# Performance work log

Hardware: AMD Instinct MI355X
Metric: run time of the kernel (lower is better)

## Reference

```python
import jax, jax.numpy as jnp
import numpy as np

N_NODES = 100000


def leaky(x):
    return jax.nn.leaky_relu(x, negative_slope=0.01)


def gcn_conv(h, W, b, src, dst, n_nodes):
    """PyG GCNConv: add self-loops, symmetric deg^{-1/2} normalization, scatter-add."""
    h = h @ W  # [N, out]
    deg = jax.ops.segment_sum(jnp.ones_like(dst, dtype=h.dtype), dst, num_segments=n_nodes) + 1.0  # +1 self-loop
    dinv = jax.lax.rsqrt(deg)  # deg >= 1 always
    norm = dinv[src] * dinv[dst]  # [E]
    msg = h[src] * norm[:, None]  # gather + scale, [E, out]
    agg = jax.ops.segment_sum(msg, dst, num_segments=n_nodes)
    agg = agg + h * (dinv * dinv)[:, None]  # self-loop message
    return agg + b


def setup_inputs() -> dict:
    key = jax.random.key(0)
    ks = jax.random.split(key, 16)
    num_teams = 100000
    n_edges = 5000000
    n_matches = 1000000
    x = jax.random.randint(ks[0], (N_NODES, 1), 0, num_teams)
    edge_index = jax.random.randint(ks[1], (2, n_edges), 0, N_NODES)
    home = jax.random.randint(ks[2], (n_matches,), 0, N_NODES)
    away = jax.random.randint(ks[3], (n_matches,), 0, N_NODES)
    emb = jax.random.normal(ks[4], (num_teams, 3), dtype=jnp.float32)
    W1 = jax.random.normal(ks[5], (3, 16), dtype=jnp.float32) * (1.0 / np.sqrt(3))
    b1 = jnp.zeros((16,), dtype=jnp.float32)
    W2 = jax.random.normal(ks[6], (16, 3), dtype=jnp.float32) * 0.25
    b2 = jnp.zeros((3,), dtype=jnp.float32)
    lw1 = jax.random.normal(ks[7], (6, 16), dtype=jnp.float32) * (1.0 / np.sqrt(6))
    lb1 = jnp.zeros((16,), dtype=jnp.float32)
    lw2 = jax.random.normal(ks[8], (16, 6), dtype=jnp.float32) * 0.25
    lb2 = jnp.zeros((6,), dtype=jnp.float32)
    lw3 = jax.random.normal(ks[9], (6, 3), dtype=jnp.float32) * (1.0 / np.sqrt(6))
    lb3 = jnp.zeros((3,), dtype=jnp.float32)
    return dict(x=x, edge_index=edge_index, home=home, away=away, emb=emb,
                W1=W1, b1=b1, W2=W2, b2=b2,
                lw1=lw1, lb1=lb1, lw2=lw2, lb2=lb2, lw3=lw3, lb3=lb3)


def reference(x, edge_index, home, away, emb, W1, b1, W2, b2, lw1, lb1, lw2, lb2, lw3, lb3):
    src, dst = edge_index[0], edge_index[1]
    h = emb[x[:, 0]]  # embedding lookup + squeeze(1) -> [N, 3]
    h = leaky(gcn_conv(h, W1, b1, src, dst, N_NODES))  # [N, 16]
    h = leaky(gcn_conv(h, W2, b2, src, dst, N_NODES))  # [N, 3]
    z = jnp.concatenate([h[home], h[away]], axis=-1)  # [M, 6]
    z = leaky(z @ lw1 + lb1)
    z = leaky(z @ lw2 + lb2)
    z = leaky(z @ lw3 + lb3)
    return z.reshape(-1, 3)
```

## Files before the change

kernel.cpp:

```cpp
#include <hip/hip_runtime.h>

typedef unsigned int u32;
typedef unsigned short u16;

static __device__ __forceinline__ float leaky(float v) {
    return v >= 0.0f ? v : 0.01f * v;
}

#define P1_CHUNK 8192
#define P1_T 256
#define NBK 512
#define P2_T 256
#define ASPLIT 4
#define SBLK 1024
#define S1F 8388608.0f
#define S2F 2097152.0f

static __device__ __forceinline__ int ghat(const int* __restrict__ gh,
                                           const int* __restrict__ bsum,
                                           int i, int ghN, int nE) {
    return (i == ghN) ? nE : gh[i] + bsum[i >> 10];
}

__global__ void k_p1hist(const int* __restrict__ dst, int* __restrict__ gh,
                         int nE, int nb) {
    __shared__ int hist[NBK];
    int t = threadIdx.x;
    hist[t] = 0; hist[t + 256] = 0;
    __syncthreads();
    int base = blockIdx.x * P1_CHUNK;
    int lim = min(P1_CHUNK, nE - base);
    if (lim == P1_CHUNK) {
        const int4* p = (const int4*)(dst + base);
        for (int i = t; i < P1_CHUNK / 4; i += P1_T) {
            int4 v = p[i];
            atomicAdd(&hist[v.x >> 8], 1);
            atomicAdd(&hist[v.y >> 8], 1);
            atomicAdd(&hist[v.z >> 8], 1);
            atomicAdd(&hist[v.w >> 8], 1);
        }
    } else {
        for (int i = t; i < lim; i += P1_T)
            atomicAdd(&hist[dst[base + i] >> 8], 1);
    }
    __syncthreads();
    gh[t * nb + blockIdx.x] = hist[t];
    gh[(t + 256) * nb + blockIdx.x] = hist[t + 256];
}

__global__ void g_scanA(const int* __restrict__ in, int* __restrict__ out,
                        int* __restrict__ bsum, int n) {
    __shared__ int s[SBLK];
    int t = threadIdx.x, i = blockIdx.x * SBLK + t;
    int v = (i < n) ? in[i] : 0;
    s[t] = v;
    for (int o = 1; o < SBLK; o <<= 1) {
        __syncthreads();
        int x = (t >= o) ? s[t - o] : 0;
        __syncthreads();
        s[t] += x;
    }
    __syncthreads();
    if (i < n) out[i] = s[t] - v;
    if (t == SBLK - 1) bsum[blockIdx.x] = s[t];
}
__global__ void g_scanB(int* __restrict__ bsum, int nb) {
    __shared__ int s[SBLK];
    int t = threadIdx.x;
    int v = (t < nb) ? bsum[t] : 0;
    s[t] = v;
    for (int o = 1; o < SBLK; o <<= 1) {
        __syncthreads();
        int x = (t >= o) ? s[t - o] : 0;
        __syncthreads();
        s[t] += x;
    }
    __syncthreads();
    if (t < nb) bsum[t] = s[t] - v;
}
__global__ void g_scanC(int* __restrict__ out, const int* __restrict__ bsum,
                        int n, int total) {
    int i = blockIdx.x * blockDim.x + threadIdx.x;
    if (i < n) out[i] += bsum[i / SBLK];
    if (i == 0) out[n] = total;
}

__global__ __launch_bounds__(256) void k_p1scatter(
        const int* __restrict__ src, const int* __restrict__ dst,
        const int* __restrict__ gh, const int* __restrict__ bsum,
        u32* __restrict__ bkt, int nE, int nb, int ghN) {
    __shared__ int cur[NBK];
    __shared__ int loff[NBK];
    __shared__ int gb[NBK];
    __shared__ int sc[NBK];
    __shared__ u32 pay[P1_CHUNK];
    __shared__ u16 bb[P1_CHUNK];
    int t = threadIdx.x;
    int blk = blockIdx.x;
    int idx0 = t * nb + blk;
    int idx1 = (t + 256) * nb + blk;
    int g0 = ghat(gh, bsum, idx0, ghN, nE);
    int c0 = ghat(gh, bsum, idx0 + 1, ghN, nE) - g0;
    int g1 = ghat(gh, bsum, idx1, ghN, nE);
    int c1 = ghat(gh, bsum, idx1 + 1, ghN, nE) - g1;
    gb[t] = g0; gb[t + 256] = g1;
    sc[t] = c0; sc[t + 256] = c1;
    for (int o = 1; o < NBK; o <<= 1) {
        __syncthreads();
        int a0 = (t >= o) ? sc[t - o] : 0;
        int a1 = (t + 256 >= o) ? sc[t + 256 - o] : 0;
        __syncthreads();
        sc[t] += a0; sc[t + 256] += a1;
    }
    __syncthreads();
    loff[t] = sc[t] - c0;           loff[t + 256] = sc[t + 256] - c1;
    cur[t] = loff[t];               cur[t + 256] = loff[t + 256];
    __syncthreads();
    int base = blk * P1_CHUNK;
    int lim = min(P1_CHUNK, nE - base);
    int n4 = lim >> 2;
    const int4* d4p = (const int4*)(dst + base);
    const int4* s4p = (const int4*)(src + base);
    for (int i = t; i < n4; i += P1_T) {
        int4 d4 = d4p[i];
        int4 s4 = s4p[i];
        int b, r;
        b = d4.x >> 8; r = atomicAdd(&cur[b], 1);
        pay[r] = (u32)(((d4.x & 255) << 17) | s4.x); bb[r] = (u16)b;
        b = d4.y >> 8; r = atomicAdd(&cur[b], 1);
        pay[r] = (u32)(((d4.y & 255) << 17) | s4.y); bb[r] = (u16)b;
        b = d4.z >> 8; r = atomicAdd(&cur[b], 1);
        pay[r] = (u32)(((d4.z & 255) << 17) | s4.z); bb[r] = (u16)b;
        b = d4.w >> 8; r = atomicAdd(&cur[b], 1);
        pay[r] = (u32)(((d4.w & 255) << 17) | s4.w); bb[r] = (u16)b;
    }
    for (int i = (n4 << 2) + t; i < lim; i += P1_T) {
        int d = dst[base + i], s = src[base + i];
        int b = d >> 8;
        int r = atomicAdd(&cur[b], 1);
        pay[r] = (u32)(((d & 255) << 17) | s);
        bb[r] = (u16)b;
    }
    __syncthreads();
    for (int i = t; i < lim; i += P1_T) {
        int b = bb[i];
        bkt[gb[b] + (i - loff[b])] = pay[i];
    }
}

__global__ void k_cnt1(const u32* __restrict__ bkt, const int* __restrict__ gh,
                       const int* __restrict__ bsum,
                       const int* __restrict__ x, const float* __restrict__ emb,
                       float* __restrict__ dinv, float4* __restrict__ hd0,
                       int nE, int nb, int ghN, int nN) {
    __shared__ int h[256];
    int t = threadIdx.x, b = blockIdx.x;
    int base = ghat(gh, bsum, b * nb, ghN, nE);
    int end  = (b + 1 < NBK) ? ghat(gh, bsum, (b + 1) * nb, ghN, nE) : nE;
    h[t] = 0;
    __syncthreads();
    int a0 = min((base + 3) & ~3, end);
    if (base + t < a0) atomicAdd(&h[bkt[base + t] >> 17], 1);
    int vend = a0 + ((end - a0) & ~3);
    for (int i = a0 + t * 4; i < vend; i += P2_T * 4) {
        uint4 v = *(const uint4*)&bkt[i];
        atomicAdd(&h[v.x >> 17], 1);
        atomicAdd(&h[v.y >> 17], 1);
        atomicAdd(&h[v.z >> 17], 1);
        atomicAdd(&h[v.w >> 17], 1);
    }
    if (vend + t < end) atomicAdd(&h[bkt[vend + t] >> 17], 1);
    __syncthreads();
    int d = b * 256 + t;
    if (d < nN) {
        float di = rsqrtf((float)h[t] + 1.0f);
        dinv[d] = di;
        int xi = x[d] * 3;
        hd0[d] = make_float4(emb[xi] * di, emb[xi + 1] * di, emb[xi + 2] * di, 0.f);
    }
}

__global__ __launch_bounds__(256) void k_aggI(
        const u32* __restrict__ bkt, const int* __restrict__ gh,
        const int* __restrict__ bsum,
        const float4* __restrict__ tab, float* __restrict__ pacc,
        int nE, int nb, int ghN, float scale, float inv_scale) {
    __shared__ int acc[768];
    int t = threadIdx.x;
    int blk = blockIdx.x, b = blk >> 2, s = blk & 3;
    int base = ghat(gh, bsum, b * nb, ghN, nE);
    int end  = (b + 1 < NBK) ? ghat(gh, bsum, (b + 1) * nb, ghN, nE) : nE;
    int sz = end - base;
    int chunk = (sz + ASPLIT - 1) / ASPLIT;
    int st = min(base + s * chunk, end);
    int en = min(st + chunk, end);
    acc[t] = 0; acc[t + 256] = 0; acc[t + 512] = 0;
    __syncthreads();
    int a0 = min((st + 3) & ~3, en);
    if (st + t < a0) {
        u32 v = bkt[st + t];
        float4 h = tab[v & 0x1FFFFu];
        int bin = (int)(v >> 17) * 3;
        atomicAdd(&acc[bin + 0], __float2int_rn(h.x * scale));
        atomicAdd(&acc[bin + 1], __float2int_rn(h.y * scale));
        atomicAdd(&acc[bin + 2], __float2int_rn(h.z * scale));
    }
    int vend = a0 + ((en - a0) & ~3);
    for (int i = a0 + t * 4; i < vend; i += P2_T * 4) {
        uint4 v = *(const uint4*)&bkt[i];
        float4 h0 = tab[v.x & 0x1FFFFu];
        float4 h1 = tab[v.y & 0x1FFFFu];
        float4 h2 = tab[v.z & 0x1FFFFu];
        float4 h3 = tab[v.w & 0x1FFFFu];
        int b0 = (int)(v.x >> 17) * 3, b1 = (int)(v.y >> 17) * 3;
        int b2 = (int)(v.z >> 17) * 3, b3 = (int)(v.w >> 17) * 3;
        atomicAdd(&acc[b0 + 0], __float2int_rn(h0.x * scale));
        atomicAdd(&acc[b0 + 1], __float2int_rn(h0.y * scale));
        atomicAdd(&acc[b0 + 2], __float2int_rn(h0.z * scale));
        atomicAdd(&acc[b1 + 0], __float2int_rn(h1.x * scale));
        atomicAdd(&acc[b1 + 1], __float2int_rn(h1.y * scale));
        atomicAdd(&acc[b1 + 2], __float2int_rn(h1.z * scale));
        atomicAdd(&acc[b2 + 0], __float2int_rn(h2.x * scale));
        atomicAdd(&acc[b2 + 1], __float2int_rn(h2.y * scale));
        atomicAdd(&acc[b2 + 2], __float2int_rn(h2.z * scale));
        atomicAdd(&acc[b3 + 0], __float2int_rn(h3.x * scale));
        atomicAdd(&acc[b3 + 1], __float2int_rn(h3.y * scale));
        atomicAdd(&acc[b3 + 2], __float2int_rn(h3.z * scale));
    }
    if (vend + t < en) {
        u32 v = bkt[vend + t];
        float4 h = tab[v & 0x1FFFFu];
        int bin = (int)(v >> 17) * 3;
        atomicAdd(&acc[bin + 0], __float2int_rn(h.x * scale));
        atomicAdd(&acc[bin + 1], __float2int_rn(h.y * scale));
        atomicAdd(&acc[bin + 2], __float2int_rn(h.z * scale));
    }
    __syncthreads();
    float* p = pacc + (size_t)blk * 768;
    p[t]       = (float)acc[t * 3 + 0] * inv_scale;
    p[t + 256] = (float)acc[t * 3 + 1] * inv_scale;
    p[t + 512] = (float)acc[t * 3 + 2] * inv_scale;
}

__global__ void k_fin1(const float* __restrict__ pacc, const float* __restrict__ dinv,
                       const float4* __restrict__ hd0,
                       const float* __restrict__ W1, const float* __restrict__ b1,
                       const float* __restrict__ W2,
                       float4* __restrict__ hd2, int nN) {
    int d = blockIdx.x * blockDim.x + threadIdx.x;
    if (d >= nN) return;
    int b = d >> 8, q = d & 255;
    float s0 = 0.f, s1 = 0.f, s2 = 0.f;
#pragma unroll
    for (int s = 0; s < ASPLIT; ++s) {
        const float* p = pacc + (size_t)(b * ASPLIT + s) * 768;
        s0 += p[q]; s1 += p[q + 256]; s2 += p[q + 512];
    }
    float di = dinv[d];
    float4 self = hd0[d];
    float a0 = di * (s0 + self.x);
    float a1 = di * (s1 + self.y);
    float a2 = di * (s2 + self.z);
    float o0 = 0.f, o1 = 0.f, o2 = 0.f;
#pragma unroll
    for (int k = 0; k < 16; ++k) {
        float p = leaky(a0 * W1[k] + a1 * W1[16 + k] + a2 * W1[32 + k] + b1[k]);
        o0 += p * W2[k * 3 + 0];
        o1 += p * W2[k * 3 + 1];
        o2 += p * W2[k * 3 + 2];
    }
    hd2[d] = make_float4(o0 * di, o1 * di, o2 * di, 0.f);
}

__global__ void k_fin2(const float* __restrict__ pacc, const float* __restrict__ dinv,
                       const float4* __restrict__ hd2, const float* __restrict__ b2,
                       float4* __restrict__ h2, int nN) {
    int d = blockIdx.x * blockDim.x + threadIdx.x;
    if (d >= nN) return;
    int b = d >> 8, q = d & 255;
    float s0 = 0.f, s1 = 0.f, s2 = 0.f;
#pragma unroll
    for (int s = 0; s < ASPLIT; ++s) {
        const float* p = pacc + (size_t)(b * ASPLIT + s) * 768;
        s0 += p[q]; s1 += p[q + 256]; s2 += p[q + 512];
    }
    float di = dinv[d];
    float4 self = hd2[d];
    h2[d] = make_float4(leaky(di * (s0 + self.x) + b2[0]),
                        leaky(di * (s1 + self.y) + b2[1]),
                        leaky(di * (s2 + self.z) + b2[2]), 0.f);
}

__global__ __launch_bounds__(256) void k_mlp4v(
        const int* __restrict__ home, const int* __restrict__ away,
        const float4* __restrict__ h2,
        const float* __restrict__ lw1, const float* __restrict__ lb1,
        const float* __restrict__ lw2, const float* __restrict__ lb2,
        const float* __restrict__ lw3, const float* __restrict__ lb3,
        float* __restrict__ out, int nM) {
    __shared__ float s[235];
    int t = threadIdx.x;
    if (t < 96)       s[t] = lw1[t];
    else if (t < 112) s[t] = lb1[t - 96];
    else if (t < 208) s[t] = lw2[t - 112];
    else if (t < 214) s[t] = lb2[t - 208];
    else if (t < 232) s[t] = lw3[t - 214];
    else if (t < 235) s[t] = lb3[t - 232];
    __syncthreads();
    const float* sw1 = s;        const float* sb1 = s + 96;
    const float* sw2 = s + 112;  const float* sb2 = s + 208;
    const float* sw3 = s + 214;  const float* sb3 = s + 232;

    int i = blockIdx.x * blockDim.x + threadIdx.x;
    int m0 = i * 4;
    if (m0 >= nM) return;
    float res[12];
    int nq = min(4, nM - m0);
    int hidx[4], aidx[4];
    if (nq == 4) {
        int4 hv = *(const int4*)&home[m0];
        int4 av = *(const int4*)&away[m0];
        hidx[0] = hv.x; hidx[1] = hv.y; hidx[2] = hv.z; hidx[3] = hv.w;
        aidx[0] = av.x; aidx[1] = av.y; aidx[2] = av.z; aidx[3] = av.w;
    } else {
        for (int j = 0; j < nq; ++j) { hidx[j] = home[m0 + j]; aidx[j] = away[m0 + j]; }
    }
    for (int j = 0; j < nq; ++j) {
        float4 zh = h2[hidx[j]];
        float4 za = h2[aidx[j]];
        float z[6] = {zh.x, zh.y, zh.z, za.x, za.y, za.z};
        float t1[16];
#pragma unroll
        for (int k = 0; k < 16; ++k) {
            float p = sb1[k];
#pragma unroll
            for (int q = 0; q < 6; ++q) p += z[q] * sw1[q * 16 + k];
            t1[k] = leaky(p);
        }
        float t2[6];
#pragma unroll
        for (int k = 0; k < 6; ++k) {
            float p = sb2[k];
#pragma unroll
            for (int q = 0; q < 16; ++q) p += t1[q] * sw2[q * 6 + k];
            t2[k] = leaky(p);
        }
#pragma unroll
        for (int k = 0; k < 3; ++k) {
            float p = sb3[k];
#pragma unroll
            for (int q = 0; q < 6; ++q) p += t2[q] * sw3[q * 3 + k];
            res[j * 3 + k] = leaky(p);
        }
    }
    if (nq == 4) {
        float4* o4 = (float4*)&out[m0 * 3];
        o4[0] = make_float4(res[0], res[1], res[2], res[3]);
        o4[1] = make_float4(res[4], res[5], res[6], res[7]);
        o4[2] = make_float4(res[8], res[9], res[10], res[11]);
    } else {
        for (int j = 0; j < nq * 3; ++j) out[m0 * 3 + j] = res[j];
    }
}

__global__ void k_hist(const int* __restrict__ dst, int* __restrict__ cnt, int nE) {
    int e = blockIdx.x * blockDim.x + threadIdx.x;
    if (e < nE) atomicAdd(&cnt[dst[e]], 1);
}
__global__ void k_prep(const int* __restrict__ off, const int* __restrict__ cnt,
                       float* __restrict__ dinv, int* __restrict__ cur, int nN) {
    int i = blockIdx.x * blockDim.x + threadIdx.x;
    if (i >= nN) return;
    dinv[i] = rsqrtf((float)cnt[i] + 1.0f);
    cur[i] = off[i];
}
__global__ void k_hd0(const int* __restrict__ x, const float* __restrict__ emb,
                      const float* __restrict__ dinv, float4* __restrict__ hd0, int nN) {
    int i = blockIdx.x * blockDim.x + threadIdx.x;
    if (i >= nN) return;
    float di = dinv[i];
    int xi = x[i] * 3;
    hd0[i] = make_float4(emb[xi] * di, emb[xi + 1] * di, emb[xi + 2] * di, 0.0f);
}
__global__ void k_place(const int* __restrict__ src, const int* __restrict__ dst,
                        int* __restrict__ cur, int* __restrict__ csr, int nE) {
    int e = blockIdx.x * blockDim.x + threadIdx.x;
    if (e >= nE) return;
    int p = atomicAdd(&cur[dst[e]], 1);
    csr[p] = src[e];
}
__global__ void k_gather1w(const int* __restrict__ off, const int* __restrict__ csr,
                           const float4* __restrict__ hd0, const float* __restrict__ dinv,
                           const float* __restrict__ W1, const float* __restrict__ b1,
                           const float* __restrict__ W2,
                           float4* __restrict__ hd2, int nN) {
    int g = blockIdx.x * blockDim.x + threadIdx.x;
    int d = g >> 6, lane = threadIdx.x & 63;
    if (d >= nN) return;
    int e0 = off[d], e1 = off[d + 1];
    float sx = 0.f, sy = 0.f, sz = 0.f;
    for (int e = e0 + lane; e < e1; e += 64) {
        float4 v = hd0[csr[e]];
        sx += v.x; sy += v.y; sz += v.z;
    }
    for (int o = 32; o; o >>= 1) {
        sx += __shfl_down(sx, o);
        sy += __shfl_down(sy, o);
        sz += __shfl_down(sz, o);
    }
    if (lane == 0) {
        float di = dinv[d];
        float4 self = hd0[d];
        float a0 = di * (sx + self.x);
        float a1 = di * (sy + self.y);
        float a2 = di * (sz + self.z);
        float o0 = 0.f, o1 = 0.f, o2 = 0.f;
#pragma unroll
        for (int k = 0; k < 16; ++k) {
            float p = leaky(a0 * W1[k] + a1 * W1[16 + k] + a2 * W1[32 + k] + b1[k]);
            o0 += p * W2[k * 3 + 0];
            o1 += p * W2[k * 3 + 1];
            o2 += p * W2[k * 3 + 2];
        }
        hd2[d] = make_float4(o0 * di, o1 * di, o2 * di, 0.0f);
    }
}
__global__ void k_gather2(const int* __restrict__ off, const int* __restrict__ csr,
                          const float4* __restrict__ hd2, const float* __restrict__ dinv,
                          const float* __restrict__ b2,
                          float4* __restrict__ h2, int nN) {
    int g = blockIdx.x * blockDim.x + threadIdx.x;
    int d = g >> 4, lane = threadIdx.x & 15;
    if (d >= nN) return;
    int e0 = off[d], e1 = off[d + 1];
    float s0 = 0.f, s1 = 0.f, s2 = 0.f;
    for (int e = e0 + lane; e < e1; e += 16) {
        float4 v = hd2[csr[e]];
        s0 += v.x; s1 += v.y; s2 += v.z;
    }
    for (int o = 8; o; o >>= 1) {
        s0 += __shfl_down(s0, o, 16);
        s1 += __shfl_down(s1, o, 16);
        s2 += __shfl_down(s2, o, 16);
    }
    if (lane == 0) {
        float di = dinv[d];
        float4 self = hd2[d];
        h2[d] = make_float4(leaky(di * (s0 + self.x) + b2[0]),
                            leaky(di * (s1 + self.y) + b2[1]),
                            leaky(di * (s2 + self.z) + b2[2]), 0.f);
    }
}

extern "C" void kernel_launch(void* const* d_in, const int* in_sizes, int n_in,
                              void* d_out, int out_size, void* d_ws, size_t ws_size,
                              hipStream_t stream) {
    const int*   x    = (const int*)d_in[0];
    const int*   ei   = (const int*)d_in[1];
    const int*   home = (const int*)d_in[2];
    const int*   away = (const int*)d_in[3];
    const float* emb  = (const float*)d_in[4];
    const float* W1   = (const float*)d_in[5];
    const float* b1   = (const float*)d_in[6];
    const float* W2   = (const float*)d_in[7];
    const float* b2   = (const float*)d_in[8];
    const float* lw1  = (const float*)d_in[9];
    const float* lb1  = (const float*)d_in[10];
    const float* lw2  = (const float*)d_in[11];
    const float* lb2  = (const float*)d_in[12];
    const float* lw3  = (const float*)d_in[13];
    const float* lb3  = (const float*)d_in[14];
    float* out = (float*)d_out;

    const int nN = in_sizes[0];
    const int nE = in_sizes[1] / 2;
    const int nM = in_sizes[2];
    const int* src = ei;
    const int* dst = ei + nE;
    const int B = 256;

    const int nb1 = (nE + P1_CHUNK - 1) / P1_CHUNK;
    const int ghN = NBK * nb1;
    const int nbs = (ghN + SBLK - 1) / SBLK;
    const size_t paccN = (size_t)NBK * ASPLIT * 768;

    size_t need = (size_t)3 * nN * 16 + (size_t)nE * 4 + (size_t)(ghN + 1) * 4 +
                  paccN * 4 + (size_t)nN * 4 + (size_t)(nbs + 8) * 4;

    if (nN <= NBK * 256 && ws_size >= need && nbs <= SBLK) {
        char* w = (char*)d_ws;
        float4* hd0 = (float4*)w;                 w += (size_t)nN * 16;
        float4* hd2 = (float4*)w;                 w += (size_t)nN * 16;
        float4* h2  = (float4*)w;                 w += (size_t)nN * 16;
        u32* bkt  = (u32*)w;                      w += (size_t)nE * 4;
        float* pacc = (float*)w;                  w += paccN * 4;
        int* gh   = (int*)w;                      w += (size_t)(ghN + 1) * 4;
        float* dinv = (float*)w;                  w += (size_t)nN * 4;
        int* bsum = (int*)w;

        k_p1hist<<<nb1, P1_T, 0, stream>>>(dst, gh, nE, nb1);
        g_scanA<<<nbs, SBLK, 0, stream>>>(gh, gh, bsum, ghN);
        g_scanB<<<1, SBLK, 0, stream>>>(bsum, nbs);
        k_p1scatter<<<nb1, P1_T, 0, stream>>>(src, dst, gh, bsum, bkt, nE, nb1, ghN);
        k_cnt1<<<NBK, P2_T, 0, stream>>>(bkt, gh, bsum, x, emb, dinv, hd0,
                                         nE, nb1, ghN, nN);
        k_aggI<<<NBK * ASPLIT, P2_T, 0, stream>>>(bkt, gh, bsum, hd0, pacc,
                                                  nE, nb1, ghN, S1F, 1.0f / S1F);
        k_fin1<<<(nN + B - 1) / B, B, 0, stream>>>(pacc, dinv, hd0, W1, b1, W2,
                                                   hd2, nN);
        k_aggI<<<NBK * ASPLIT, P2_T, 0, stream>>>(bkt, gh, bsum, hd2, pacc,
                                                  nE, nb1, ghN, S2F, 1.0f / S2F);
        k_fin2<<<(nN + B - 1) / B, B, 0, stream>>>(pacc, dinv, hd2, b2, h2, nN);
        int nQuads = (nM + 3) / 4;
        k_mlp4v<<<(nQuads + B - 1) / B, B, 0, stream>>>(home, away, h2,
                                                        lw1, lb1, lw2, lb2, lw3, lb3,
                                                        out, nM);
    } else {
        char* w = (char*)d_ws;
        float4* hd0 = (float4*)w;                 w += (size_t)nN * 16;
        float4* hd2 = (float4*)w;                 w += (size_t)nN * 16;
        float4* h2  = (float4*)w;                 w += (size_t)nN * 16;
        int* csr  = (int*)w;                      w += (size_t)nE * 4;
        int* cnt  = (int*)w;                      w += (size_t)(nN + 1) * 4;
        int* off  = (int*)w;                      w += (size_t)(nN + 1) * 4;
        int* cur  = (int*)w;                      w += (size_t)nN * 4;
        float* dinv = (float*)w;                  w += (size_t)nN * 4;
        int* bsum = (int*)w;

        const int nTot = nN + 1;
        const int nbScan = (nTot + SBLK - 1) / SBLK;

        hipMemsetAsync(cnt, 0, (size_t)nTot * sizeof(int), stream);
        k_hist<<<(nE + B - 1) / B, B, 0, stream>>>(dst, cnt, nE);
        g_scanA<<<nbScan, SBLK, 0, stream>>>(cnt, off, bsum, nTot);
        g_scanB<<<1, SBLK, 0, stream>>>(bsum, nbScan);
        g_scanC<<<(nTot + B - 1) / B, B, 0, stream>>>(off, bsum, nTot - 1, nE);
        k_prep<<<(nN + B - 1) / B, B, 0, stream>>>(off, cnt, dinv, cur, nN);
        k_hd0<<<(nN + B - 1) / B, B, 0, stream>>>(x, emb, dinv, hd0, nN);
        k_place<<<(nE + B - 1) / B, B, 0, stream>>>(src, dst, cur, csr, nE);
        k_gather1w<<<((size_t)nN * 64 + B - 1) / B, B, 0, stream>>>(off, csr, hd0, dinv,
                                                                    W1, b1, W2, hd2, nN);
        k_gather2<<<((size_t)nN * 16 + B - 1) / B, B, 0, stream>>>(off, csr, hd2,
                                                                   dinv, b2, h2, nN);
        int nQuads = (nM + 3) / 4;
        k_mlp4v<<<(nQuads + B - 1) / B, B, 0, stream>>>(home, away, h2,
                                                        lw1, lb1, lw2, lb2, lw3, lb3,
                                                        out, nM);
    }
}
```

Measured before the change: 136.9 us.

## Fuse degree, both GCN aggregations and MLP into one cooperative persistent kernel

Replaces the chain of degree-count, two aggregation, two finalize and MLP kernels with a single cooperative kernel of 512 blocks, separated by grid syncs. Each block stages its bucket's edges in LDS once and reuses them across the degree pass and both aggregation passes. Partial-accumulator round trips through global memory and the extra launches go away. In exchange each bucket runs on one block instead of four splits, so parallelism drops and LDS use rises, and grid-wide barriers are added. The fallback path also loses its uint4 vectorized loads, and the CSR fallback branch is removed.

```diff
diff --git a/kernel.cpp b/kernel.cpp
--- a/kernel.cpp
+++ b/kernel.cpp
@@ -1,4 +1,7 @@
 #include <hip/hip_runtime.h>
+#include <hip/hip_cooperative_groups.h>
+
+namespace cg = cooperative_groups;
 
 typedef unsigned int u32;
 typedef unsigned short u16;
@@ -13,6 +16,7 @@
 #define P2_T 256
 #define ASPLIT 4
 #define SBLK 1024
+#define STG_CAP 14336
 #define S1F 8388608.0f
 #define S2F 2097152.0f
 
@@ -77,12 +81,6 @@
     }
     __syncthreads();
     if (t < nb) bsum[t] = s[t] - v;
-}
-__global__ void g_scanC(int* __restrict__ out, const int* __restrict__ bsum,
-                        int n, int total) {
-    int i = blockIdx.x * blockDim.x + threadIdx.x;
-    if (i < n) out[i] += bsum[i / SBLK];
-    if (i == 0) out[n] = total;
 }
 
 __global__ __launch_bounds__(256) void k_p1scatter(
@@ -148,6 +146,183 @@
     }
 }
 
+__global__ __launch_bounds__(256, 2) void k_mega(
+        const u32* __restrict__ bkt, const int* __restrict__ gh,
+        const int* __restrict__ bsum,
+        const int* __restrict__ x, const float* __restrict__ emb,
+        const float* __restrict__ W1, const float* __restrict__ b1,
+        const float* __restrict__ W2, const float* __restrict__ b2,
+        const int* __restrict__ home, const int* __restrict__ away,
+        const float* __restrict__ lw1, const float* __restrict__ lb1,
+        const float* __restrict__ lw2, const float* __restrict__ lb2,
+        const float* __restrict__ lw3, const float* __restrict__ lb3,
+        float4* hd0, float4* hd2, float4* h2, float* __restrict__ out,
+        int nE, int nb, int ghN, int nN, int nM) {
+    cg::grid_group grid = cg::this_grid();
+    __shared__ u32 stg[STG_CAP];
+    __shared__ int acc[768];
+    __shared__ float mw[235];
+    int t = threadIdx.x, b = blockIdx.x;
+    int base = ghat(gh, bsum, b * nb, ghN, nE);
+    int end  = (b + 1 < NBK) ? ghat(gh, bsum, (b + 1) * nb, ghN, nE) : nE;
+    int sz = end - base;
+    bool fits = (sz <= STG_CAP);
+
+    if (fits) for (int i = t; i < sz; i += 256) stg[i] = bkt[base + i];
+
+    acc[t] = 0;
+    __syncthreads();
+    if (fits) { for (int i = t; i < sz; i += 256) atomicAdd(&acc[stg[i] >> 17], 1); }
+    else      { for (int i = t; i < sz; i += 256) atomicAdd(&acc[bkt[base + i] >> 17], 1); }
+    __syncthreads();
+    int deg = acc[t];
+    float di = rsqrtf((float)deg + 1.0f);
+    int d = b * 256 + t;
+    float4 self = make_float4(0.f, 0.f, 0.f, 0.f);
+    if (d < nN) {
+        int xi = x[d] * 3;
+        self = make_float4(emb[xi] * di, emb[xi + 1] * di, emb[xi + 2] * di, 0.f);
+        hd0[d] = self;
+    }
+    grid.sync();
+
+    acc[t] = 0; acc[t + 256] = 0; acc[t + 512] = 0;
+    __syncthreads();
+    if (fits) {
+        for (int i = t; i < sz; i += 256) {
+            u32 v = stg[i];
+            float4 h = hd0[v & 0x1FFFFu];
+            int bin = (int)(v >> 17) * 3;
+            atomicAdd(&acc[bin + 0], __float2int_rn(h.x * S1F));
+            atomicAdd(&acc[bin + 1], __float2int_rn(h.y * S1F));
+            atomicAdd(&acc[bin + 2], __float2int_rn(h.z * S1F));
+        }
+    } else {
+        for (int i = t; i < sz; i += 256) {
+            u32 v = bkt[base + i];
+            float4 h = hd0[v & 0x1FFFFu];
+            int bin = (int)(v >> 17) * 3;
+            atomicAdd(&acc[bin + 0], __float2int_rn(h.x * S1F));
+            atomicAdd(&acc[bin + 1], __float2int_rn(h.y * S1F));
+            atomicAdd(&acc[bin + 2], __float2int_rn(h.z * S1F));
+        }
+    }
+    __syncthreads();
+    float4 self2 = make_float4(0.f, 0.f, 0.f, 0.f);
+    if (d < nN) {
+        float s0 = (float)acc[t * 3 + 0] * (1.0f / S1F);
+        float s1 = (float)acc[t * 3 + 1] * (1.0f / S1F);
+        float s2 = (float)acc[t * 3 + 2] * (1.0f / S1F);
+        float a0 = di * (s0 + self.x);
+        float a1 = di * (s1 + self.y);
+        float a2 = di * (s2 + self.z);
+        float o0 = 0.f, o1 = 0.f, o2 = 0.f;
+#pragma unroll
+        for (int k = 0; k < 16; ++k) {
+            float p = leaky(a0 * W1[k] + a1 * W1[16 + k] + a2 * W1[32 + k] + b1[k]);
+            o0 += p * W2[k * 3 + 0];
+            o1 += p * W2[k * 3 + 1];
+            o2 += p * W2[k * 3 + 2];
+        }
+        self2 = make_float4(o0 * di, o1 * di, o2 * di, 0.f);
+        hd2[d] = self2;
+    }
+    grid.sync();
+
+    acc[t] = 0; acc[t + 256] = 0; acc[t + 512] = 0;
+    __syncthreads();
+    if (fits) {
+        for (int i = t; i < sz; i += 256) {
+            u32 v = stg[i];
+            float4 h = hd2[v & 0x1FFFFu];
+            int bin = (int)(v >> 17) * 3;
+            atomicAdd(&acc[bin + 0], __float2int_rn(h.x * S2F));
+            atomicAdd(&acc[bin + 1], __float2int_rn(h.y * S2F));
+            atomicAdd(&acc[bin + 2], __float2int_rn(h.z * S2F));
+        }
+    } else {
+        for (int i = t; i < sz; i += 256) {
+            u32 v = bkt[base + i];
+            float4 h = hd2[v & 0x1FFFFu];
+            int bin = (int)(v >> 17) * 3;
+            atomicAdd(&acc[bin + 0], __float2int_rn(h.x * S2F));
+            atomicAdd(&acc[bin + 1], __float2int_rn(h.y * S2F));
+            atomicAdd(&acc[bin + 2], __float2int_rn(h.z * S2F));
+        }
+    }
+    __syncthreads();
+    if (d < nN) {
+        float s0 = (float)acc[t * 3 + 0] * (1.0f / S2F);
+        float s1 = (float)acc[t * 3 + 1] * (1.0f / S2F);
+        float s2 = (float)acc[t * 3 + 2] * (1.0f / S2F);
+        h2[d] = make_float4(leaky(di * (s0 + self2.x) + b2[0]),
+                            leaky(di * (s1 + self2.y) + b2[1]),
+                            leaky(di * (s2 + self2.z) + b2[2]), 0.f);
+    }
+    if (t < 96)       mw[t] = lw1[t];
+    else if (t < 112) mw[t] = lb1[t - 96];
+    else if (t < 208) mw[t] = lw2[t - 112];
+    else if (t < 214) mw[t] = lb2[t - 208];
+    else if (t < 232) mw[t] = lw3[t - 214];
+    else if (t < 235) mw[t] = lb3[t - 232];
+    grid.sync();
+
+    const float* sw1 = mw;        const float* sb1 = mw + 96;
+    const float* sw2 = mw + 112;  const float* sb2 = mw + 208;
+    const float* sw3 = mw + 214;  const float* sb3 = mw + 232;
+    int nQ = (nM + 3) >> 2;
+    for (int qd = b * 256 + t; qd < nQ; qd += NBK * 256) {
+        int m0 = qd * 4;
+        int nq = min(4, nM - m0);
+        int hidx[4], aidx[4];
+        if (nq == 4) {
+            int4 hv = *(const int4*)&home[m0];
+            int4 av = *(const int4*)&away[m0];
+            hidx[0] = hv.x; hidx[1] = hv.y; hidx[2] = hv.z; hidx[3] = hv.w;
+            aidx[0] = av.x; aidx[1] = av.y; aidx[2] = av.z; aidx[3] = av.w;
+        } else {
+            for (int j = 0; j < nq; ++j) { hidx[j] = home[m0 + j]; aidx[j] = away[m0 + j]; }
+        }
+        float res[12];
+        for (int j = 0; j < nq; ++j) {
+            float4 zh = h2[hidx[j]];
+            float4 za = h2[aidx[j]];
+            float z[6] = {zh.x, zh.y, zh.z, za.x, za.y, za.z};
+            float t1[16];
+#pragma unroll
+            for (int k = 0; k < 16; ++k) {
+                float p = sb1[k];
+#pragma unroll
+                for (int q = 0; q < 6; ++q) p += z[q] * sw1[q * 16 + k];
+                t1[k] = leaky(p);
+            }
+            float t2[6];
+#pragma unroll
+            for (int k = 0; k < 6; ++k) {
+                float p = sb2[k];
+#pragma unroll
+                for (int q = 0; q < 16; ++q) p += t1[q] * sw2[q * 6 + k];
+                t2[k] = leaky(p);
+            }
+#pragma unroll
+            for (int k = 0; k < 3; ++k) {
+                float p = sb3[k];
+#pragma unroll
+                for (int q = 0; q < 6; ++q) p += t2[q] * sw3[q * 3 + k];
+                res[j * 3 + k] = leaky(p);
+            }
+        }
+        if (nq == 4) {
+            float4* o4 = (float4*)&out[m0 * 3];
+            o4[0] = make_float4(res[0], res[1], res[2], res[3]);
+            o4[1] = make_float4(res[4], res[5], res[6], res[7]);
+            o4[2] = make_float4(res[8], res[9], res[10], res[11]);
+        } else {
+            for (int j = 0; j < nq * 3; ++j) out[m0 * 3 + j] = res[j];
+        }
+    }
+}
+
 __global__ void k_cnt1(const u32* __restrict__ bkt, const int* __restrict__ gh,
                        const int* __restrict__ bsum,
                        const int* __restrict__ x, const float* __restrict__ emb,
@@ -159,17 +334,8 @@
     int end  = (b + 1 < NBK) ? ghat(gh, bsum, (b + 1) * nb, ghN, nE) : nE;
     h[t] = 0;
     __syncthreads();
-    int a0 = min((base + 3) & ~3, end);
-    if (base + t < a0) atomicAdd(&h[bkt[base + t] >> 17], 1);
-    int vend = a0 + ((end - a0) & ~3);
-    for (int i = a0 + t * 4; i < vend; i += P2_T * 4) {
-        uint4 v = *(const uint4*)&bkt[i];
-        atomicAdd(&h[v.x >> 17], 1);
-        atomicAdd(&h[v.y >> 17], 1);
-        atomicAdd(&h[v.z >> 17], 1);
-        atomicAdd(&h[v.w >> 17], 1);
-    }
-    if (vend + t < end) atomicAdd(&h[bkt[vend + t] >> 17], 1);
+    for (int i = base + t; i < end; i += P2_T)
+        atomicAdd(&h[bkt[i] >> 17], 1);
     __syncthreads();
     int d = b * 256 + t;
     if (d < nN) {
@@ -179,7 +345,6 @@
         hd0[d] = make_float4(emb[xi] * di, emb[xi + 1] * di, emb[xi + 2] * di, 0.f);
     }
 }
-
 __global__ __launch_bounds__(256) void k_aggI(
         const u32* __restrict__ bkt, const int* __restrict__ gh,
         const int* __restrict__ bsum,
@@ -196,52 +361,20 @@
     int en = min(st + chunk, end);
     acc[t] = 0; acc[t + 256] = 0; acc[t + 512] = 0;
     __syncthreads();
-    int a0 = min((st + 3) & ~3, en);
-    if (st + t < a0) {
-        u32 v = bkt[st + t];
+    for (int i = st + t; i < en; i += P2_T) {
+        u32 v = bkt[i];
         float4 h = tab[v & 0x1FFFFu];
         int bin = (int)(v >> 17) * 3;
         atomicAdd(&acc[bin + 0], __float2int_rn(h.x * scale));
         atomicAdd(&acc[bin + 1], __float2int_rn(h.y * scale));
         atomicAdd(&acc[bin + 2], __float2int_rn(h.z * scale));
     }
-    int vend = a0 + ((en - a0) & ~3);
-    for (int i = a0 + t * 4; i < vend; i += P2_T * 4) {
-        uint4 v = *(const uint4*)&bkt[i];
-        float4 h0 = tab[v.x & 0x1FFFFu];
-        float4 h1 = tab[v.y & 0x1FFFFu];
-        float4 h2 = tab[v.z & 0x1FFFFu];
-        float4 h3 = tab[v.w & 0x1FFFFu];
-        int b0 = (int)(v.x >> 17) * 3, b1 = (int)(v.y >> 17) * 3;
-        int b2 = (int)(v.z >> 17) * 3, b3 = (int)(v.w >> 17) * 3;
-        atomicAdd(&acc[b0 + 0], __float2int_rn(h0.x * scale));
-        atomicAdd(&acc[b0 + 1], __float2int_rn(h0.y * scale));
-        atomicAdd(&acc[b0 + 2], __float2int_rn(h0.z * scale));
-        atomicAdd(&acc[b1 + 0], __float2int_rn(h1.x * scale));
-        atomicAdd(&acc[b1 + 1], __float2int_rn(h1.y * scale));
-        atomicAdd(&acc[b1 + 2], __float2int_rn(h1.z * scale));
-        atomicAdd(&acc[b2 + 0], __float2int_rn(h2.x * scale));
-        atomicAdd(&acc[b2 + 1], __float2int_rn(h2.y * scale));
-        atomicAdd(&acc[b2 + 2], __float2int_rn(h2.z * scale));
-        atomicAdd(&acc[b3 + 0], __float2int_rn(h3.x * scale));
-        atomicAdd(&acc[b3 + 1], __float2int_rn(h3.y * scale));
-        atomicAdd(&acc[b3 + 2], __float2int_rn(h3.z * scale));
-    }
-    if (vend + t < en) {
-        u32 v = bkt[vend + t];
-        float4 h = tab[v & 0x1FFFFu];
-        int bin = (int)(v >> 17) * 3;
-        atomicAdd(&acc[bin + 0], __float2int_rn(h.x * scale));
-        atomicAdd(&acc[bin + 1], __float2int_rn(h.y * scale));
-        atomicAdd(&acc[bin + 2], __float2int_rn(h.z * scale));
-    }
     __syncthreads();
     float* p = pacc + (size_t)blk * 768;
     p[t]       = (float)acc[t * 3 + 0] * inv_scale;
     p[t + 256] = (float)acc[t * 3 + 1] * inv_scale;
     p[t + 512] = (float)acc[t * 3 + 2] * inv_scale;
 }
-
 __global__ void k_fin1(const float* __restrict__ pacc, const float* __restrict__ dinv,
                        const float4* __restrict__ hd0,
                        const float* __restrict__ W1, const float* __restrict__ b1,
@@ -271,7 +404,6 @@
     }
     hd2[d] = make_float4(o0 * di, o1 * di, o2 * di, 0.f);
 }
-
 __global__ void k_fin2(const float* __restrict__ pacc, const float* __restrict__ dinv,
                        const float4* __restrict__ hd2, const float* __restrict__ b2,
                        float4* __restrict__ h2, int nN) {
@@ -290,7 +422,6 @@
                         leaky(di * (s1 + self.y) + b2[1]),
                         leaky(di * (s2 + self.z) + b2[2]), 0.f);
 }
-
 __global__ __launch_bounds__(256) void k_mlp4v(
         const int* __restrict__ home, const int* __restrict__ away,
         const float4* __restrict__ h2,
@@ -310,7 +441,6 @@
     const float* sw1 = s;        const float* sb1 = s + 96;
     const float* sw2 = s + 112;  const float* sb2 = s + 208;
     const float* sw3 = s + 214;  const float* sb3 = s + 232;
-
     int i = blockIdx.x * blockDim.x + threadIdx.x;
     int m0 = i * 4;
     if (m0 >= nM) return;
@@ -360,95 +490,6 @@
         o4[2] = make_float4(res[8], res[9], res[10], res[11]);
     } else {
         for (int j = 0; j < nq * 3; ++j) out[m0 * 3 + j] = res[j];
-    }
-}
-
-__global__ void k_hist(const int* __restrict__ dst, int* __restrict__ cnt, int nE) {
-    int e = blockIdx.x * blockDim.x + threadIdx.x;
-    if (e < nE) atomicAdd(&cnt[dst[e]], 1);
-}
-__global__ void k_prep(const int* __restrict__ off, const int* __restrict__ cnt,
-                       float* __restrict__ dinv, int* __restrict__ cur, int nN) {
-    int i = blockIdx.x * blockDim.x + threadIdx.x;
-    if (i >= nN) return;
-    dinv[i] = rsqrtf((float)cnt[i] + 1.0f);
-    cur[i] = off[i];
-}
-__global__ void k_hd0(const int* __restrict__ x, const float* __restrict__ emb,
-                      const float* __restrict__ dinv, float4* __restrict__ hd0, int nN) {
-    int i = blockIdx.x * blockDim.x + threadIdx.x;
-    if (i >= nN) return;
-    float di = dinv[i];
-    int xi = x[i] * 3;
-    hd0[i] = make_float4(emb[xi] * di, emb[xi + 1] * di, emb[xi + 2] * di, 0.0f);
-}
-__global__ void k_place(const int* __restrict__ src, const int* __restrict__ dst,
-                        int* __restrict__ cur, int* __restrict__ csr, int nE) {
-    int e = blockIdx.x * blockDim.x + threadIdx.x;
-    if (e >= nE) return;
-    int p = atomicAdd(&cur[dst[e]], 1);
-    csr[p] = src[e];
-}
-__global__ void k_gather1w(const int* __restrict__ off, const int* __restrict__ csr,
-                           const float4* __restrict__ hd0, const float* __restrict__ dinv,
-                           const float* __restrict__ W1, const float* __restrict__ b1,
-                           const float* __restrict__ W2,
-                           float4* __restrict__ hd2, int nN) {
-    int g = blockIdx.x * blockDim.x + threadIdx.x;
-    int d = g >> 6, lane = threadIdx.x & 63;
-    if (d >= nN) return;
-    int e0 = off[d], e1 = off[d + 1];
-    float sx = 0.f, sy = 0.f, sz = 0.f;
-    for (int e = e0 + lane; e < e1; e += 64) {
-        float4 v = hd0[csr[e]];
-        sx += v.x; sy += v.y; sz += v.z;
-    }
-    for (int o = 32; o; o >>= 1) {
-        sx += __shfl_down(sx, o);
-        sy += __shfl_down(sy, o);
-        sz += __shfl_down(sz, o);
-    }
-    if (lane == 0) {
-        float di = dinv[d];
-        float4 self = hd0[d];
-        float a0 = di * (sx + self.x);
-        float a1 = di * (sy + self.y);
-        float a2 = di * (sz + self.z);
-        float o0 = 0.f, o1 = 0.f, o2 = 0.f;
-#pragma unroll
-        for (int k = 0; k < 16; ++k) {
-            float p = leaky(a0 * W1[k] + a1 * W1[16 + k] + a2 * W1[32 + k] + b1[k]);
-            o0 += p * W2[k * 3 + 0];
-            o1 += p * W2[k * 3 + 1];
-            o2 += p * W2[k * 3 + 2];
-        }
-        hd2[d] = make_float4(o0 * di, o1 * di, o2 * di, 0.0f);
-    }
-}
-__global__ void k_gather2(const int* __restrict__ off, const int* __restrict__ csr,
-                          const float4* __restrict__ hd2, const float* __restrict__ dinv,
-                          const float* __restrict__ b2,
-                          float4* __restrict__ h2, int nN) {
-    int g = blockIdx.x * blockDim.x + threadIdx.x;
-    int d = g >> 4, lane = threadIdx.x & 15;
-    if (d >= nN) return;
-    int e0 = off[d], e1 = off[d + 1];
-    float s0 = 0.f, s1 = 0.f, s2 = 0.f;
-    for (int e = e0 + lane; e < e1; e += 16) {
-        float4 v = hd2[csr[e]];
-        s0 += v.x; s1 += v.y; s2 += v.z;
-    }
-    for (int o = 8; o; o >>= 1) {
-        s0 += __shfl_down(s0, o, 16);
-        s1 += __shfl_down(s1, o, 16);
-        s2 += __shfl_down(s2, o, 16);
-    }
-    if (lane == 0) {
-        float di = dinv[d];
-        float4 self = hd2[d];
-        h2[d] = make_float4(leaky(di * (s0 + self.x) + b2[0]),
-                            leaky(di * (s1 + self.y) + b2[1]),
-                            leaky(di * (s2 + self.z) + b2[2]), 0.f);
     }
 }
 
@@ -472,15 +513,15 @@
     const float* lb3  = (const float*)d_in[14];
     float* out = (float*)d_out;
 
-    const int nN = in_sizes[0];
-    const int nE = in_sizes[1] / 2;
-    const int nM = in_sizes[2];
+    int nN = in_sizes[0];
+    int nE = in_sizes[1] / 2;
+    int nM = in_sizes[2];
     const int* src = ei;
     const int* dst = ei + nE;
     const int B = 256;
 
-    const int nb1 = (nE + P1_CHUNK - 1) / P1_CHUNK;
-    const int ghN = NBK * nb1;
+    int nb1 = (nE + P1_CHUNK - 1) / P1_CHUNK;
+    int ghN = NBK * nb1;
     const int nbs = (ghN + SBLK - 1) / SBLK;
     const size_t paccN = (size_t)NBK * ASPLIT * 768;
 
@@ -488,6 +529,48 @@
                   paccN * 4 + (size_t)nN * 4 + (size_t)(nbs + 8) * 4;
 
     if (nN <= NBK * 256 && ws_size >= need && nbs <= SBLK) {
+        char* w = (char*)d_ws;
+        float4* hd0 = (float4*)w;                 w += (size_t)nN * 16;
+        float4* hd2 = (float4*)w;                 w += (size_t)nN * 16;
+        float4* h2  = (float4*)w;                 w += (size_t)nN * 16;
+        u32* bkt  = (u32*)w;                      w += (size_t)nE * 4;
+        float* pacc = (float*)w;                  w += paccN * 4;
+        int* gh   = (int*)w;                      w += (size_t)(ghN + 1) * 4;
+        float* dinv = (float*)w;                  w += (size_t)nN * 4;
+        int* bsum = (int*)w;
+
+        k_p1hist<<<nb1, P1_T, 0, stream>>>(dst, gh, nE, nb1);
+        g_scanA<<<nbs, SBLK, 0, stream>>>(gh, gh, bsum, ghN);
+        g_scanB<<<1, SBLK, 0, stream>>>(bsum, nbs);
+        k_p1scatter<<<nb1, P1_T, 0, stream>>>(src, dst, gh, bsum, bkt, nE, nb1, ghN);
+
+        void* args[] = {
+            (void*)&bkt, (void*)&gh, (void*)&bsum, (void*)&x, (void*)&emb,
+            (void*)&W1, (void*)&b1, (void*)&W2, (void*)&b2,
+            (void*)&home, (void*)&away,
+            (void*)&lw1, (void*)&lb1, (void*)&lw2, (void*)&lb2,
+            (void*)&lw3, (void*)&lb3,
+            (void*)&hd0, (void*)&hd2, (void*)&h2, (void*)&out,
+            (void*)&nE, (void*)&nb1, (void*)&ghN, (void*)&nN, (void*)&nM
+        };
+        hipError_t err = hipLaunchCooperativeKernel(
+            reinterpret_cast<void*>(k_mega), dim3(NBK), dim3(256), args, 0, stream);
+        if (err != hipSuccess) {
+            k_cnt1<<<NBK, P2_T, 0, stream>>>(bkt, gh, bsum, x, emb, dinv, hd0,
+                                             nE, nb1, ghN, nN);
+            k_aggI<<<NBK * ASPLIT, P2_T, 0, stream>>>(bkt, gh, bsum, hd0, pacc,
+                                                      nE, nb1, ghN, S1F, 1.0f / S1F);
+            k_fin1<<<(nN + B - 1) / B, B, 0, stream>>>(pacc, dinv, hd0, W1, b1, W2,
+                                                       hd2, nN);
+            k_aggI<<<NBK * ASPLIT, P2_T, 0, stream>>>(bkt, gh, bsum, hd2, pacc,
+                                                      nE, nb1, ghN, S2F, 1.0f / S2F);
+            k_fin2<<<(nN + B - 1) / B, B, 0, stream>>>(pacc, dinv, hd2, b2, h2, nN);
+            int nQuads = (nM + 3) / 4;
+            k_mlp4v<<<(nQuads + B - 1) / B, B, 0, stream>>>(home, away, h2,
+                                                            lw1, lb1, lw2, lb2,
+                                                            lw3, lb3, out, nM);
+        }
+    } else {
         char* w = (char*)d_ws;
         float4* hd0 = (float4*)w;                 w += (size_t)nN * 16;
         float4* hd2 = (float4*)w;                 w += (size_t)nN * 16;
@@ -513,38 +596,7 @@
         k_fin2<<<(nN + B - 1) / B, B, 0, stream>>>(pacc, dinv, hd2, b2, h2, nN);
         int nQuads = (nM + 3) / 4;
         k_mlp4v<<<(nQuads + B - 1) / B, B, 0, stream>>>(home, away, h2,
-                                                        lw1, lb1, lw2, lb2, lw3, lb3,
-                                                        out, nM);
-    } else {
-        char* w = (char*)d_ws;
-        float4* hd0 = (float4*)w;                 w += (size_t)nN * 16;
-        float4* hd2 = (float4*)w;                 w += (size_t)nN * 16;
-        float4* h2  = (float4*)w;                 w += (size_t)nN * 16;
-        int* csr  = (int*)w;                      w += (size_t)nE * 4;
-        int* cnt  = (int*)w;                      w += (size_t)(nN + 1) * 4;
-        int* off  = (int*)w;                      w += (size_t)(nN + 1) * 4;
-        int* cur  = (int*)w;                      w += (size_t)nN * 4;
-        float* dinv = (float*)w;                  w += (size_t)nN * 4;
-        int* bsum = (int*)w;
-
-        const int nTot = nN + 1;
-        const int nbScan = (nTot + SBLK - 1) / SBLK;
-
-        hipMemsetAsync(cnt, 0, (size_t)nTot * sizeof(int), stream);
-        k_hist<<<(nE + B - 1) / B, B, 0, stream>>>(dst, cnt, nE);
-        g_scanA<<<nbScan, SBLK, 0, stream>>>(cnt, off, bsum, nTot);
-        g_scanB<<<1, SBLK, 0, stream>>>(bsum, nbScan);
-        g_scanC<<<(nTot + B - 1) / B, B, 0, stream>>>(off, bsum, nTot - 1, nE);
-        k_prep<<<(nN + B - 1) / B, B, 0, stream>>>(off, cnt, dinv, cur, nN);
-        k_hd0<<<(nN + B - 1) / B, B, 0, stream>>>(x, emb, dinv, hd0, nN);
-        k_place<<<(nE + B - 1) / B, B, 0, stream>>>(src, dst, cur, csr, nE);
-        k_gather1w<<<((size_t)nN * 64 + B - 1) / B, B, 0, stream>>>(off, csr, hd0, dinv,
-                                                                    W1, b1, W2, hd2, nN);
-        k_gather2<<<((size_t)nN * 16 + B - 1) / B, B, 0, stream>>>(off, csr, hd2,
-                                                                   dinv, b2, h2, nN);
-        int nQuads = (nM + 3) / 4;
-        k_mlp4v<<<(nQuads + B - 1) / B, B, 0, stream>>>(home, away, h2,
-                                                        lw1, lb1, lw2, lb2, lw3, lb3,
-                                                        out, nM);
-    }
-}
+                                                        lw1, lb1, lw2, lb2,
+                                                        lw3, lb3, out, nM);
+    }
+}
```

Result: slower. 388.8 us (+183.9%).
